# Kernel optimization log

Measured on AMD Instinct MI355X. Metric: run time of the kernel, lower is better.

## Reference

```python
import jax, jax.numpy as jnp
import numpy as np

CHANNELS = 64
WEIGHT_NUMS = [66 * 64, 64 * 64, 64]  # layer0 (C+2)->C, layer1 C->C, layer2 C->1
BIAS_NUMS = [64, 64, 1]
NUM_GEN_PARAMS = sum(WEIGHT_NUMS) + sum(BIAS_NUMS)  # 8513


def setup_inputs() -> dict:
    key = jax.random.key(0)
    k1, k2 = jax.random.split(key)
    N, C, H, W = 4, 64, 80, 200
    num_ins = 8  # instances per image -> M = 32 total
    M = N * num_ins
    x = jax.random.normal(k1, (N, C, H, W), dtype=jnp.float32)
    mask_head_params = jax.random.normal(k2, (M, NUM_GEN_PARAMS), dtype=jnp.float32) * 0.1
    return {"x": x, "mask_head_params": mask_head_params, "num_ins": num_ins}


def reference(x, mask_head_params, num_ins):
    N, C, H, W = x.shape
    ch = CHANNELS
    # compute_locations with stride=1 (stride//2 == 0); source bug divides the
    # whole tensor by W (locations[:1,:,:] /= W on a batch-1 tensor).
    xx, yy = jnp.meshgrid(jnp.arange(W, dtype=x.dtype), jnp.arange(H, dtype=x.dtype), indexing='xy')
    loc = jnp.stack([xx, yy], axis=0) / W  # [2, H, W]
    xa = jnp.concatenate([jnp.broadcast_to(loc[None], (N, 2, H, W)), x], axis=1)  # [N, C+2, H, W]
    feats = jnp.repeat(xa, num_ins, axis=0)  # [M, C+2, H, W] per-instance inputs
    M = feats.shape[0]
    # parse_dynamic_params: split generated params into per-layer weights/biases
    splits = np.cumsum(WEIGHT_NUMS + BIAS_NUMS)[:-1]
    w0, w1, w2, b0, b1, b2 = jnp.split(mask_head_params, splits, axis=1)
    w0 = w0.reshape(M, ch, ch + 2)
    w1 = w1.reshape(M, ch, ch)
    w2 = w2.reshape(M, 1, ch)
    b2 = b2 - 2.19  # mask bias shift (is_mask=True)
    # grouped 1x1 convs (groups=M) as per-instance GEMMs with ReLU between layers
    h = jax.nn.relu(jnp.einsum('mkc,mchw->mkhw', w0, feats) + b0[:, :, None, None])
    h = jax.nn.relu(jnp.einsum('mkc,mchw->mkhw', w1, h) + b1[:, :, None, None])
    out = jnp.einsum('mkc,mchw->mkhw', w2, h) + b2[:, :, None, None]
    return out.reshape(1, -1, H, W)  # [1, M*out_channels, H, W]
```

## Files before the change

### kernel.cpp

```cpp
#include <hip/hip_runtime.h>

typedef __attribute__((ext_vector_type(8)))  short    short8;
typedef __attribute__((ext_vector_type(4)))  short    s16x4;
typedef __attribute__((ext_vector_type(4)))  float    f32x4;
typedef __attribute__((ext_vector_type(4)))  unsigned uint4_;
typedef __attribute__((ext_vector_type(2)))  unsigned uint2_;

#define HW     16000
#define WWID   200
#define NPARAM 8513

__device__ __forceinline__ unsigned pkbf2(float a, float b) {
    unsigned r;
    asm("v_cvt_pk_bf16_f32 %0, %1, %2" : "=v"(r) : "v"(a), "v"(b));
    return r;
}
__device__ __forceinline__ short8 mk8(unsigned a, unsigned b, unsigned c, unsigned d) {
    uint4_ u; u.x = a; u.y = b; u.z = c; u.w = d;
    return __builtin_bit_cast(short8, u);
}
__device__ __forceinline__ s16x4 mk4(unsigned a, unsigned b) {
    uint2_ u; u.x = a; u.y = b;
    return __builtin_bit_cast(s16x4, u);
}
__device__ __forceinline__ void mfma16(f32x4& acc, s16x4 a, s16x4 b) {
    asm("s_nop 2\n\tv_mfma_f32_16x16x16_bf16 %0, %1, %2, %0"
        : "+v"(acc) : "v"(a), "v"(b));
}

__global__ __launch_bounds__(512, 2) void condlane_reg(
    const float* __restrict__ x,
    const float* __restrict__ params,
    float* __restrict__ out,
    int num_ins)
{
    extern __shared__ char lds_[];
    char* xt = lds_;
    const int tid  = threadIdx.x;
    const int lane = tid & 63;
    const int wid  = tid >> 6;
    const int n    = blockIdx.y;
    const int pxg0 = blockIdx.x * 256;
    const int g    = (lane >> 4) & 3;
    const int px16 = lane & 15;

    {
        const int p   = tid & 255;
        const int sel = tid >> 8;
        const int pc  = min(pxg0 + p, HW - 1);
        const float* xp = x + (size_t)n * 64 * HW + pc;
        #pragma unroll
        for (int it = 0; it < 4; ++it) {
            int c0 = sel * 32 + it * 8;
            uint4_ d;
            d.x = pkbf2(xp[(size_t)(c0 + 0) * HW], xp[(size_t)(c0 + 1) * HW]);
            d.y = pkbf2(xp[(size_t)(c0 + 2) * HW], xp[(size_t)(c0 + 3) * HW]);
            d.z = pkbf2(xp[(size_t)(c0 + 4) * HW], xp[(size_t)(c0 + 5) * HW]);
            d.w = pkbf2(xp[(size_t)(c0 + 6) * HW], xp[(size_t)(c0 + 7) * HW]);
            *(uint4_*)(xt + ((p * 256 + c0 * 2) ^ ((p & 15) << 4))) = d;
        }
        const int pg = pxg0 + p;
        float lx = (float)(pg % WWID) * (1.0f / WWID);
        float ly = (float)(pg / WWID) * (1.0f / WWID);
        uint4_ z;  z.x = 0; z.y = 0; z.z = 0; z.w = 0;
        uint4_ cv; cv.x = pkbf2(lx, ly); cv.y = pkbf2(1.f, 0.f); cv.z = 0; cv.w = 0;
        int ba = (p * 256 + 128 + sel * 32) ^ ((p & 15) << 4);
        int bb = (p * 256 + 144 + sel * 32) ^ ((p & 15) << 4);
        *(uint4_*)(xt + ba) = (sel == 0) ? cv : z;
        *(uint4_*)(xt + bb) = z;
    }

    const int m = n * num_ins + wid;
    const float* pm = params + (size_t)m * NPARAM;

    short8 w0f[3][4];
    s16x4  w1f4[4][4];
    #pragma unroll
    for (int kb = 0; kb < 4; ++kb) {
        const int k = kb * 16 + px16;
        #pragma unroll
        for (int ch = 0; ch < 2; ++ch) {
            const float* s0 = pm + k * 66 + 2 + ch * 32 + g * 8;
            w0f[ch][kb] = mk8(pkbf2(s0[0], s0[1]), pkbf2(s0[2], s0[3]),
                              pkbf2(s0[4], s0[5]), pkbf2(s0[6], s0[7]));
        }
        float a = (g == 0) ? pm[k * 66 + 0] : 0.f;
        float b = (g == 0) ? pm[k * 66 + 1] : 0.f;
        float c = (g == 0) ? pm[8384 + k]   : 0.f;
        w0f[2][kb] = mk8(pkbf2(a, b), pkbf2(c, 0.f), 0u, 0u);
        #pragma unroll
        for (int ks = 0; ks < 4; ++ks) {
            const float* s1 = pm + 4224 + (kb * 16 + px16) * 64 + ks * 16 + g * 4;
            w1f4[kb][ks] = mk4(pkbf2(s1[0], s1[1]), pkbf2(s1[2], s1[3]));
        }
    }
    f32x4 bias1[4], w2v[4];
    #pragma unroll
    for (int kb = 0; kb < 4; ++kb)
        #pragma unroll
        for (int r = 0; r < 4; ++r) {
            bias1[kb][r] = pm[8448 + kb * 16 + g * 4 + r];
            w2v[kb][r]   = pm[8320 + kb * 16 + g * 4 + r];
        }
    const float b2 = pm[8512] - 2.19f;

    __syncthreads();

    const int swz = px16 << 4;
    const int nsl = min(16, (HW - pxg0) >> 4);

    for (int s = 0; s < 16; ++s) {
        const int pxl = s * 16 + px16;
        short8 xf[3];
        #pragma unroll
        for (int ch = 0; ch < 3; ++ch)
            xf[ch] = *(const short8*)(xt + ((pxl * 256 + ch * 64 + g * 16) ^ swz));
        f32x4 acc0[4];
        #pragma unroll
        for (int kb = 0; kb < 4; ++kb)
            #pragma unroll
            for (int j = 0; j < 4; ++j) acc0[kb][j] = 0.f;
        #pragma unroll
        for (int ch = 0; ch < 3; ++ch)
            #pragma unroll
            for (int kb = 0; kb < 4; ++kb)
                acc0[kb] = __builtin_amdgcn_mfma_f32_16x16x32_bf16(w0f[ch][kb], xf[ch], acc0[kb], 0, 0, 0);
        s16x4 hf[4];
        #pragma unroll
        for (int ks = 0; ks < 4; ++ks)
            hf[ks] = mk4(pkbf2(fmaxf(acc0[ks][0], 0.f), fmaxf(acc0[ks][1], 0.f)),
                         pkbf2(fmaxf(acc0[ks][2], 0.f), fmaxf(acc0[ks][3], 0.f)));
        f32x4 acc1[4];
        #pragma unroll
        for (int kb = 0; kb < 4; ++kb) acc1[kb] = bias1[kb];
        #pragma unroll
        for (int ks = 0; ks < 4; ++ks)
            #pragma unroll
            for (int kb = 0; kb < 4; ++kb)
                mfma16(acc1[kb], w1f4[kb][ks], hf[ks]);
        asm("s_nop 7\n\ts_nop 7"
            : "+v"(acc1[0]), "+v"(acc1[1]), "+v"(acc1[2]), "+v"(acc1[3]));
        float v = 0.f;
        #pragma unroll
        for (int kb = 0; kb < 4; ++kb)
            #pragma unroll
            for (int r = 0; r < 4; ++r)
                v += w2v[kb][r] * fmaxf(acc1[kb][r], 0.f);
        v += __shfl_xor(v, 16);
        v += __shfl_xor(v, 32);
        if (lane < 16 && s < nsl)
            out[(size_t)m * HW + pxg0 + s * 16 + lane] = v + b2;
    }
}

extern "C" void kernel_launch(void* const* d_in, const int* in_sizes, int n_in,
                              void* d_out, int out_size, void* d_ws, size_t ws_size,
                              hipStream_t stream) {
    const float* x      = (const float*)d_in[0];
    const float* params = (const float*)d_in[1];
    float* out          = (float*)d_out;

    const int N = in_sizes[0] / (64 * HW);
    const int M = in_sizes[1] / NPARAM;
    const int num_ins = M / N;

    dim3 grid((HW + 255) / 256, N);
    condlane_reg<<<grid, 512, 65536, stream>>>(x, params, out, num_ins);
}
```

Measured before the change: 26.25 us.

## Prepack per-instance weights into MFMA fragment layout in a separate kernel

Adds a small pre-kernel that converts each instance's generated parameters to bf16 and stores them in the exact per-lane MFMA fragment order in workspace. The main kernel then loads weights with wide vector loads instead of many strided scalar fp32 loads plus conversions, which every block previously repeated redundantly. Launch bounds are raised to request 3 blocks per SIMD group. The trade-off is an extra kernel launch and a workspace round trip, and the occupancy hint may force register pressure or spills.

```diff
diff --git a/kernel.cpp b/kernel.cpp
--- a/kernel.cpp
+++ b/kernel.cpp
@@ -9,6 +9,7 @@
 #define HW     16000
 #define WWID   200
 #define NPARAM 8513
+#define PACK_STRIDE 6144
 
 __device__ __forceinline__ unsigned pkbf2(float a, float b) {
     unsigned r;
@@ -28,9 +29,55 @@
         : "+v"(acc) : "v"(a), "v"(b));
 }
 
-__global__ __launch_bounds__(512, 2) void condlane_reg(
+__device__ __forceinline__ float w0val(const float* pm, int k, int c) {
+    if (c < 64)  return pm[k * 66 + c + 2];
+    if (c == 64) return pm[k * 66 + 0];
+    if (c == 65) return pm[k * 66 + 1];
+    if (c == 66) return pm[8384 + k];
+    return 0.0f;
+}
+
+__global__ __launch_bounds__(256) void pack_weights(
+    const float* __restrict__ params, unsigned* __restrict__ wp)
+{
+    const int m   = blockIdx.x;
+    const int tid = threadIdx.x;
+    const float* pm = params + (size_t)m * NPARAM;
+    unsigned* dst = wp + (size_t)m * PACK_STRIDE;
+
+    if (blockIdx.y == 0) {
+        const int l  = tid >> 2;
+        const int i0 = (tid & 3) * 2;
+        #pragma unroll
+        for (int frag = 0; frag < 12; ++frag) {
+            int ch = frag >> 2, kb = frag & 3;
+            int k = kb * 16 + (l & 15);
+            int c = ch * 32 + (l >> 4) * 8 + i0;
+            dst[frag * 256 + tid] = pkbf2(w0val(pm, k, c), w0val(pm, k, c + 1));
+        }
+        float* fd = (float*)dst;
+        if (tid < 64) {
+            fd[5120 + tid] = pm[8448 + tid];
+            fd[5184 + tid] = pm[8320 + tid];
+        }
+        if (tid == 0) fd[5248] = pm[8512];
+    } else {
+        #pragma unroll
+        for (int i = tid; i < 2048; i += 256) {
+            int f = i >> 7, r = i & 127;
+            int l = r >> 1, d = i & 1;
+            int kb = f >> 2, ks = f & 3;
+            int row = kb * 16 + (l & 15);
+            int col = ks * 16 + (l >> 4) * 4 + d * 2;
+            const float* s = pm + 4224 + row * 64 + col;
+            dst[3072 + i] = pkbf2(s[0], s[1]);
+        }
+    }
+}
+
+__global__ __launch_bounds__(512, 3) void condlane_reg(
     const float* __restrict__ x,
-    const float* __restrict__ params,
+    const unsigned* __restrict__ wp,
     float* __restrict__ out,
     int num_ins)
 {
@@ -71,38 +118,28 @@
     }
 
     const int m = n * num_ins + wid;
-    const float* pm = params + (size_t)m * NPARAM;
+    const unsigned* wm = wp + (size_t)m * PACK_STRIDE;
 
     short8 w0f[3][4];
     s16x4  w1f4[4][4];
     #pragma unroll
-    for (int kb = 0; kb < 4; ++kb) {
-        const int k = kb * 16 + px16;
-        #pragma unroll
-        for (int ch = 0; ch < 2; ++ch) {
-            const float* s0 = pm + k * 66 + 2 + ch * 32 + g * 8;
-            w0f[ch][kb] = mk8(pkbf2(s0[0], s0[1]), pkbf2(s0[2], s0[3]),
-                              pkbf2(s0[4], s0[5]), pkbf2(s0[6], s0[7]));
-        }
-        float a = (g == 0) ? pm[k * 66 + 0] : 0.f;
-        float b = (g == 0) ? pm[k * 66 + 1] : 0.f;
-        float c = (g == 0) ? pm[8384 + k]   : 0.f;
-        w0f[2][kb] = mk8(pkbf2(a, b), pkbf2(c, 0.f), 0u, 0u);
-        #pragma unroll
-        for (int ks = 0; ks < 4; ++ks) {
-            const float* s1 = pm + 4224 + (kb * 16 + px16) * 64 + ks * 16 + g * 4;
-            w1f4[kb][ks] = mk4(pkbf2(s1[0], s1[1]), pkbf2(s1[2], s1[3]));
-        }
-    }
+    for (int ch = 0; ch < 3; ++ch)
+        #pragma unroll
+        for (int kb = 0; kb < 4; ++kb)
+            w0f[ch][kb] = *(const short8*)(wm + (ch * 4 + kb) * 256 + lane * 4);
+    #pragma unroll
+    for (int kb = 0; kb < 4; ++kb)
+        #pragma unroll
+        for (int ks = 0; ks < 4; ++ks)
+            w1f4[kb][ks] = *(const s16x4*)(wm + 3072 + (kb * 4 + ks) * 128 + lane * 2);
+    const float* fm = (const float*)wm;
     f32x4 bias1[4], w2v[4];
     #pragma unroll
-    for (int kb = 0; kb < 4; ++kb)
-        #pragma unroll
-        for (int r = 0; r < 4; ++r) {
-            bias1[kb][r] = pm[8448 + kb * 16 + g * 4 + r];
-            w2v[kb][r]   = pm[8320 + kb * 16 + g * 4 + r];
-        }
-    const float b2 = pm[8512] - 2.19f;
+    for (int kb = 0; kb < 4; ++kb) {
+        bias1[kb] = *(const f32x4*)(fm + 5120 + kb * 16 + g * 4);
+        w2v[kb]   = *(const f32x4*)(fm + 5184 + kb * 16 + g * 4);
+    }
+    const float b2 = fm[5248] - 2.19f;
 
     __syncthreads();
 
@@ -164,6 +201,8 @@
     const int M = in_sizes[1] / NPARAM;
     const int num_ins = M / N;
 
+    pack_weights<<<dim3(M, 2), 256, 0, stream>>>(params, (unsigned*)d_ws);
+
     dim3 grid((HW + 255) / 256, N);
-    condlane_reg<<<grid, 512, 65536, stream>>>(x, params, out, num_ins);
-}
+    condlane_reg<<<grid, 512, 65536, stream>>>(x, (const unsigned*)d_ws, out, num_ins);
+}
```

Result: slower. 26.85 us (+2.3%).
